# Kernel optimization log

Hardware: AMD Instinct MI355X
Metric: run time of the kernel (lower is better)

## Reference

```python
import jax, jax.numpy as jnp
import numpy as np

HEADS = 8
DIM_HEAD = 64
DIM = 512
MAX_POS_EMB = 512
SCALE = DIM_HEAD ** -0.5


def setup_inputs() -> dict:
    key = jax.random.key(0)
    ks = jax.random.split(key, 6)
    B, N = 2, 2048
    inner = HEADS * DIM_HEAD  # 512
    x = jax.random.normal(ks[0], (B, N, DIM), dtype=jnp.float32)
    # torch Linear weights stored as [out, in]; we keep [in, out] for x @ W
    Wq = jax.random.normal(ks[1], (DIM, inner), dtype=jnp.float32) * (DIM ** -0.5)
    Wkv = jax.random.normal(ks[2], (DIM, 2 * inner), dtype=jnp.float32) * (DIM ** -0.5)
    Wo = jax.random.normal(ks[3], (inner, DIM), dtype=jnp.float32) * (inner ** -0.5)
    bo = jax.random.normal(ks[4], (DIM,), dtype=jnp.float32) * 0.02
    rel_emb = jax.random.normal(ks[5], (2 * MAX_POS_EMB + 1, DIM_HEAD), dtype=jnp.float32)
    return {"x": x, "Wq": Wq, "Wkv": Wkv, "Wo": Wo, "bo": bo, "rel_emb": rel_emb}


def reference(x, Wq, Wkv, Wo, bo, rel_emb):
    B, N, _ = x.shape
    h, d = HEADS, DIM_HEAD
    q = x @ Wq                                # [B, N, h*d]
    kv = x @ Wkv                              # [B, N, 2*h*d]
    k, v = jnp.split(kv, 2, axis=-1)
    to_heads = lambda t: t.reshape(B, N, h, d).transpose(0, 2, 1, 3)  # [B, h, N, d]
    q, k, v = to_heads(q), to_heads(k), to_heads(v)

    dots = jnp.einsum('bhid,bhjd->bhij', q, k) * SCALE  # [B, h, N, N]

    # relative positional bias: dist clamped to [-max, max], shifted to [0, 2*max]
    seq = jnp.arange(N)
    dist = jnp.clip(seq[:, None] - seq[None, :], -MAX_POS_EMB, MAX_POS_EMB) + MAX_POS_EMB
    rel = rel_emb[dist]                                 # [N, N, d]
    pos_attn = jnp.einsum('bhnd,njd->bhnj', q, rel) * SCALE
    dots = dots + pos_attn

    attn = jax.nn.softmax(dots, axis=-1)
    out = jnp.einsum('bhij,bhjd->bhid', attn, v)        # [B, h, N, d]
    out = out.transpose(0, 2, 1, 3).reshape(B, N, h * d)
    return out @ Wo + bo
```

## Files before the change

kernel.cpp:

```cpp
#include <hip/hip_runtime.h>
#include <hip/hip_bf16.h>
#include <stdint.h>

#define HEADS 8
#define DHEAD 64
#define DIM 512
#define NSEQ 2048
#define BATCH 2
#define NROWS (BATCH * NSEQ)
#define QKV_N 1536
#define REL_ROWS 1025
#define REL_PITCH 1088
#define NSPLIT 2
#define KV_PER_SPLIT (NSEQ / NSPLIT)

static constexpr float SCALE_LOG2E = 0.125f * 1.4426950408889634f;

typedef __attribute__((ext_vector_type(8))) short bf16x8;
typedef __attribute__((ext_vector_type(4))) float f32x4;

__device__ __forceinline__ uint16_t f2bf(float f) {
    union { float f; uint32_t u; } v{f};
    uint32_t r = (v.u + 0x7FFFu + ((v.u >> 16) & 1u)) >> 16;
    return (uint16_t)r;
}
__device__ __forceinline__ float bf2f(uint16_t u) {
    union { uint32_t u; float f; } v{(uint32_t)u << 16};
    return v.f;
}

__global__ void prep_misc(const float* __restrict__ x, const float* __restrict__ rel,
                          uint16_t* __restrict__ xb, uint16_t* __restrict__ relb) {
    int total = NROWS * DIM + REL_PITCH * DHEAD;
    for (int idx = blockIdx.x * blockDim.x + threadIdx.x; idx < total; idx += gridDim.x * blockDim.x) {
        if (idx < NROWS * DIM) {
            xb[idx] = f2bf(x[idx]);
        } else {
            int i2 = idx - NROWS * DIM;
            relb[i2] = (i2 < REL_ROWS * DHEAD) ? f2bf(rel[i2]) : (uint16_t)0;
        }
    }
}

__global__ void prep_w(const float* __restrict__ Wq, const float* __restrict__ Wkv,
                       const float* __restrict__ Wo,
                       uint16_t* __restrict__ Wqkv_t, uint16_t* __restrict__ Wo_t) {
    __shared__ float tile[32][33];
    int bid = blockIdx.x;
    const float* src; uint16_t* dst; int J, ti, tj;
    if (bid < 256)      { src = Wq;  dst = Wqkv_t;             J = 512;  ti = bid >> 4;        tj = bid & 15; }
    else if (bid < 768) { int b = bid - 256; src = Wkv; dst = Wqkv_t + 512 * 512; J = 1024; ti = b >> 5; tj = b & 31; }
    else                { int b = bid - 768; src = Wo;  dst = Wo_t;   J = 512;  ti = b >> 4;        tj = b & 15; }
    int tx = threadIdx.x & 31, ty = threadIdx.x >> 5;
    int k0 = ti * 32, j0 = tj * 32;
    #pragma unroll
    for (int i = 0; i < 4; i++) tile[ty + 8 * i][tx] = src[(size_t)(k0 + ty + 8 * i) * J + j0 + tx];
    __syncthreads();
    #pragma unroll
    for (int i = 0; i < 4; i++) dst[(size_t)(j0 + ty + 8 * i) * 512 + k0 + tx] = f2bf(tile[tx][ty + 8 * i]);
}

template <bool BF16_OUT>
__global__ __launch_bounds__(256) void gemm128(const uint16_t* __restrict__ A,
                                               const uint16_t* __restrict__ Bt,
                                               void* __restrict__ Cout,
                                               const float* __restrict__ bias,
                                               int K, int ldc) {
    __shared__ char lds[32768];
    char* ldsA = lds;
    char* ldsB = lds + 16384;
    int m0 = blockIdx.x * 128, n0 = blockIdx.y * 128;
    int t = threadIdx.x, lane = t & 63, w = t >> 6;
    int wr = w >> 1, wc = w & 1;
    int l15 = lane & 15, lh = lane >> 4;
    f32x4 acc[4][4] = {};
    for (int k0 = 0; k0 < K; k0 += 64) {
        __syncthreads();
        {
            int row = t >> 3, ch = t & 7;
            #pragma unroll
            for (int p = 0; p < 4; p++) {
                int r = row + 32 * p;
                bf16x8 va = *(const bf16x8*)(A + (size_t)(m0 + r) * K + k0 + ch * 8);
                *(bf16x8*)(ldsA + r * 128 + ((ch * 16) ^ ((r & 7) << 4))) = va;
                bf16x8 vb = *(const bf16x8*)(Bt + (size_t)(n0 + r) * K + k0 + ch * 8);
                *(bf16x8*)(ldsB + r * 128 + ((ch * 16) ^ ((r & 7) << 4))) = vb;
            }
        }
        __syncthreads();
        #pragma unroll
        for (int kk = 0; kk < 2; kk++) {
            bf16x8 a[4], b[4];
            #pragma unroll
            for (int mi = 0; mi < 4; mi++) {
                int m = wr * 64 + mi * 16 + l15;
                a[mi] = *(const bf16x8*)(ldsA + m * 128 + ((kk * 64 + lh * 16) ^ ((m & 7) << 4)));
            }
            #pragma unroll
            for (int ni = 0; ni < 4; ni++) {
                int n = wc * 64 + ni * 16 + l15;
                b[ni] = *(const bf16x8*)(ldsB + n * 128 + ((kk * 64 + lh * 16) ^ ((n & 7) << 4)));
            }
            #pragma unroll
            for (int mi = 0; mi < 4; mi++)
                #pragma unroll
                for (int ni = 0; ni < 4; ni++)
                    acc[mi][ni] = __builtin_amdgcn_mfma_f32_16x16x32_bf16(a[mi], b[ni], acc[mi][ni], 0, 0, 0);
        }
    }
    #pragma unroll
    for (int mi = 0; mi < 4; mi++)
        #pragma unroll
        for (int ni = 0; ni < 4; ni++)
            #pragma unroll
            for (int i = 0; i < 4; i++) {
                int m = m0 + wr * 64 + mi * 16 + lh * 4 + i;
                int n = n0 + wc * 64 + ni * 16 + l15;
                float v = acc[mi][ni][i];
                if constexpr (BF16_OUT) ((uint16_t*)Cout)[(size_t)m * ldc + n] = f2bf(v);
                else                    ((float*)Cout)[(size_t)m * ldc + n] = v + bias[n];
            }
}

__global__ __launch_bounds__(256) void qrel_gemm(const uint16_t* __restrict__ QKV,
                                                 const uint16_t* __restrict__ relb,
                                                 uint16_t* __restrict__ qrel) {
    __shared__ char lds[16384];
    char* ldsA = lds;
    char* ldsB = lds + 8192;
    int h = blockIdx.y;
    int r0 = blockIdx.x * 64;
    int t = threadIdx.x, lane = t & 63, w = t >> 6;
    int l15 = lane & 15, lh = lane >> 4;
    {
        int row = t >> 3, ch = t & 7;
        #pragma unroll
        for (int p = 0; p < 2; p++) {
            int r = row + 32 * p;
            bf16x8 v = *(const bf16x8*)(QKV + (size_t)(r0 + r) * QKV_N + h * 64 + ch * 8);
            *(bf16x8*)(ldsA + r * 128 + ((ch * 16) ^ ((r & 7) << 4))) = v;
        }
    }
    __syncthreads();
    bf16x8 afrag[2];
    #pragma unroll
    for (int kk = 0; kk < 2; kk++) {
        int m = w * 16 + l15;
        afrag[kk] = *(const bf16x8*)(ldsA + m * 128 + ((kk * 64 + lh * 16) ^ ((m & 7) << 4)));
    }
    for (int pb = 0; pb < REL_PITCH / 64; pb++) {
        int p0 = pb * 64;
        __syncthreads();
        {
            int row = t >> 3, ch = t & 7;
            #pragma unroll
            for (int p = 0; p < 2; p++) {
                int r = row + 32 * p;
                bf16x8 v = *(const bf16x8*)(relb + (size_t)(p0 + r) * 64 + ch * 8);
                *(bf16x8*)(ldsB + r * 128 + ((ch * 16) ^ ((r & 7) << 4))) = v;
            }
        }
        __syncthreads();
        f32x4 acc[4] = {};
        #pragma unroll
        for (int kk = 0; kk < 2; kk++)
            #pragma unroll
            for (int ni = 0; ni < 4; ni++) {
                int n = ni * 16 + l15;
                bf16x8 b = *(const bf16x8*)(ldsB + n * 128 + ((kk * 64 + lh * 16) ^ ((n & 7) << 4)));
                acc[ni] = __builtin_amdgcn_mfma_f32_16x16x32_bf16(afrag[kk], b, acc[ni], 0, 0, 0);
            }
        #pragma unroll
        for (int ni = 0; ni < 4; ni++)
            #pragma unroll
            for (int i = 0; i < 4; i++) {
                int rr = r0 + w * 16 + lh * 4 + i;
                int p = p0 + ni * 16 + l15;
                qrel[((size_t)h * NROWS + rr) * REL_PITCH + p] = f2bf(acc[ni][i]);
            }
    }
}

__global__ __launch_bounds__(512, 4) void attn_kernel(const uint16_t* __restrict__ QKV,
                                                      const uint16_t* __restrict__ qrel,
                                                      float* __restrict__ Opart,
                                                      float* __restrict__ mlpart) {
    __shared__ char lds[53248];
    char* ldsQ = lds;
    char* ldsKV = lds + 16384;
    int qb = blockIdx.x, h = blockIdx.y;
    int b = blockIdx.z >> 1, sp = blockIdx.z & 1;
    int t = threadIdx.x, lane = t & 63, w = t >> 6;
    int l15 = lane & 15, lh = lane >> 4;
    int row = t >> 3, ch = t & 7;
    int n0 = qb * 128;
    int kvbase = sp * KV_PER_SPLIT;
    size_t rowQ = (size_t)b * NSEQ + n0;

    {
        int buf = t >> 8, idx = t & 255;
        uint32_t val = (idx < 16) ? 0x3F803F80u : 0u;
        char* p = ldsKV + buf * 18432 + 8192 + 8192 + (idx >> 4) * 128 + (idx & 15) * 8;
        *(uint32_t*)(p) = val;
        *(uint32_t*)(p + 4) = val;
    }

    #pragma unroll
    for (int p = 0; p < 2; p++) {
        int r = row + 64 * p;
        bf16x8 v = *(const bf16x8*)(QKV + (rowQ + r) * QKV_N + h * 64 + ch * 8);
        *(bf16x8*)(ldsQ + r * 128 + ((ch * 16) ^ ((r & 7) << 4))) = v;
    }
    __syncthreads();
    bf16x8 qf[2];
    #pragma unroll
    for (int kk = 0; kk < 2; kk++) {
        int m = w * 16 + l15;
        qf[kk] = *(const bf16x8*)(ldsQ + m * 128 + ((kk * 64 + lh * 16) ^ ((m & 7) << 4)));
    }
    char* myP = ldsQ + w * 2048;

    f32x4 oacc[5] = {};
    float mrow[4];
    #pragma unroll
    for (int i = 0; i < 4; i++) mrow[i] = -INFINITY;

    const uint16_t* qbase = qrel + ((size_t)h * NROWS + (size_t)b * NSEQ) * REL_PITCH;
    uint32_t rowbase[4];
    #pragma unroll
    for (int i = 0; i < 4; i++) rowbase[i] = (uint32_t)(n0 + w * 16 + lh * 4 + i) * REL_PITCH + 512;

    auto load_kv = [&](int tile, bf16x8& kr, bf16x8& vr) {
        size_t gro = ((size_t)b * NSEQ + kvbase + tile * 64 + row) * QKV_N + h * 64 + ch * 8;
        kr = *(const bf16x8*)(QKV + gro + 512);
        vr = *(const bf16x8*)(QKV + gro + 1024);
    };
    auto scatter_kv = [&](int tile, bf16x8& kr, bf16x8& vr) {
        char* ldsK = ldsKV + (tile & 1) * 18432;
        char* ldsV = ldsK + 8192;
        *(bf16x8*)(ldsK + row * 128 + ((ch * 16) ^ ((row & 7) << 4))) = kr;
        #pragma unroll
        for (int dd = 0; dd < 8; dd++) {
            int d = ch * 8 + dd;
            int s = dd ^ ch;
            *(uint16_t*)(ldsV + d * 128 + 2 * (row ^ (s << 3))) = (uint16_t)vr[dd];
        }
    };
    auto load_g = [&](int tile, uint16_t* g) {
        int kv0 = kvbase + tile * 64;
        int rel0 = n0 - kv0;
        if (rel0 <= -640) {
            #pragma unroll
            for (int i = 0; i < 4; i++) {
                uint16_t v = qbase[rowbase[i] - 512];
                #pragma unroll
                for (int nf = 0; nf < 4; nf++) g[nf * 4 + i] = v;
            }
        } else if (rel0 >= 576) {
            #pragma unroll
            for (int i = 0; i < 4; i++) {
                uint16_t v = qbase[rowbase[i] + 512];
                #pragma unroll
                for (int nf = 0; nf < 4; nf++) g[nf * 4 + i] = v;
            }
        } else {
            #pragma unroll
            for (int i = 0; i < 4; i++) {
                int nmk = (n0 + w * 16 + lh * 4 + i) - kv0;
                #pragma unroll
                for (int nf = 0; nf < 4; nf++) {
                    int d = nmk - (nf * 16 + l15);
                    d = d < -512 ? -512 : (d > 512 ? 512 : d);
                    g[nf * 4 + i] = qbase[rowbase[i] + d];
                }
            }
        }
    };

    const int NT = KV_PER_SPLIT / 64;
    uint16_t gA[16], gB[16];
    bf16x8 kreg, vreg;
    load_kv(0, kreg, vreg);
    load_g(0, gA);
    scatter_kv(0, kreg, vreg);

    auto body = [&](int tt, uint16_t* gCur, uint16_t* gNext) {
        char* ldsK = ldsKV + (tt & 1) * 18432;
        char* ldsV = ldsK + 8192;
        __syncthreads();
        bool pf = (tt + 1 < NT);
        if (pf) { load_kv(tt + 1, kreg, vreg); load_g(tt + 1, gNext); }

        f32x4 sacc[4] = {};
        __builtin_amdgcn_s_setprio(1);
        #pragma unroll
        for (int kk = 0; kk < 2; kk++)
            #pragma unroll
            for (int nf = 0; nf < 4; nf++) {
                int n = nf * 16 + l15;
                bf16x8 kfv = *(const bf16x8*)(ldsK + n * 128 + ((kk * 64 + lh * 16) ^ ((n & 7) << 4)));
                sacc[nf] = __builtin_amdgcn_mfma_f32_16x16x32_bf16(qf[kk], kfv, sacc[nf], 0, 0, 0);
            }
        __builtin_amdgcn_s_setprio(0);

        #pragma unroll
        for (int nf = 0; nf < 4; nf++)
            #pragma unroll
            for (int i = 0; i < 4; i++)
                sacc[nf][i] += bf2f(gCur[nf * 4 + i]);

        float lmax = sacc[0][0];
        #pragma unroll
        for (int nf = 0; nf < 4; nf++)
            #pragma unroll
            for (int i = 0; i < 4; i++) lmax = fmaxf(lmax, sacc[nf][i]);
        float mmin = fminf(fminf(mrow[0], mrow[1]), fminf(mrow[2], mrow[3]));
        if (!__all(lmax <= mmin + 64.0f)) {
            #pragma unroll
            for (int i = 0; i < 4; i++) {
                float mx = fmaxf(fmaxf(sacc[0][i], sacc[1][i]), fmaxf(sacc[2][i], sacc[3][i]));
                mx = fmaxf(mx, __shfl_xor(mx, 1));
                mx = fmaxf(mx, __shfl_xor(mx, 2));
                mx = fmaxf(mx, __shfl_xor(mx, 4));
                mx = fmaxf(mx, __shfl_xor(mx, 8));
                float mnew = fmaxf(mrow[i], mx);
                float alpha = exp2f((mrow[i] - mnew) * SCALE_LOG2E);
                mrow[i] = mnew;
                #pragma unroll
                for (int nf = 0; nf < 5; nf++) oacc[nf][i] *= alpha;
            }
        }

        #pragma unroll
        for (int i = 0; i < 4; i++) {
            int r = lh * 4 + i;
            int rsw = (r & 7) << 4;
            #pragma unroll
            for (int nf = 0; nf < 4; nf++) {
                float p = exp2f((sacc[nf][i] - mrow[i]) * SCALE_LOG2E);
                uint32_t pb;
                asm("v_cvt_pk_bf16_f32 %0, %1, %2" : "=v"(pb) : "v"(p), "v"(p));
                *(uint16_t*)(myP + r * 128 + (((nf * 16 + l15) * 2) ^ rsw)) = (uint16_t)pb;
            }
        }

        asm volatile("s_waitcnt lgkmcnt(0)" ::: "memory");
        __builtin_amdgcn_s_setprio(1);
        #pragma unroll
        for (int kk = 0; kk < 2; kk++) {
            bf16x8 pa = *(const bf16x8*)(myP + l15 * 128 + ((kk * 64 + lh * 16) ^ ((l15 & 7) << 4)));
            #pragma unroll
            for (int nf = 0; nf < 5; nf++) {
                int d = nf * 16 + l15;
                int sd = (d & 7) ^ ((d >> 3) & 7);
                bf16x8 vb = *(const bf16x8*)(ldsV + d * 128 + 16 * ((kk * 4 + lh) ^ sd));
                oacc[nf] = __builtin_amdgcn_mfma_f32_16x16x32_bf16(pa, vb, oacc[nf], 0, 0, 0);
            }
        }
        __builtin_amdgcn_s_setprio(0);
        if (pf) scatter_kv(tt + 1, kreg, vreg);
    };

    #pragma unroll 1
    for (int tt2 = 0; tt2 < NT; tt2 += 2) {
        body(tt2, gA, gB);
        body(tt2 + 1, gB, gA);
    }

    size_t rbase = ((size_t)(sp * BATCH + b) * HEADS + h) * NSEQ;
    #pragma unroll
    for (int nf = 0; nf < 4; nf++)
        #pragma unroll
        for (int i = 0; i < 4; i++) {
            int r = n0 + w * 16 + lh * 4 + i;
            Opart[(rbase + r) * 64 + nf * 16 + l15] = oacc[nf][i];
        }
    if (l15 == 0) {
        #pragma unroll
        for (int i = 0; i < 4; i++) {
            int r = n0 + w * 16 + lh * 4 + i;
            mlpart[(rbase + r) * 2]     = mrow[i];
            mlpart[(rbase + r) * 2 + 1] = oacc[4][i];
        }
    }
}

__global__ __launch_bounds__(256) void combine_kernel(const float* __restrict__ Opart,
                                                      const float* __restrict__ mlpart,
                                                      uint16_t* __restrict__ attO) {
    int lane = threadIdx.x & 63;
    int R = blockIdx.x * 4 + (threadIdx.x >> 6);
    const int SPSTRIDE = BATCH * HEADS * NSEQ;
    float m1 = mlpart[(size_t)R * 2], l1 = mlpart[(size_t)R * 2 + 1];
    float m2 = mlpart[((size_t)SPSTRIDE + R) * 2], l2 = mlpart[((size_t)SPSTRIDE + R) * 2 + 1];
    float M = fmaxf(m1, m2);
    float w1 = exp2f((m1 - M) * SCALE_LOG2E);
    float w2 = exp2f((m2 - M) * SCALE_LOG2E);
    float Linv = 1.f / (l1 * w1 + l2 * w2);
    float o1 = Opart[(size_t)R * 64 + lane];
    float o2 = Opart[((size_t)SPSTRIDE + R) * 64 + lane];
    float o = (o1 * w1 + o2 * w2) * Linv;
    int bh = R >> 11, n = R & 2047;
    int b = bh >> 3, hh = bh & 7;
    attO[((size_t)(b * NSEQ + n)) * DIM + hh * 64 + lane] = f2bf(o);
}

extern "C" void kernel_launch(void* const* d_in, const int* in_sizes, int n_in,
                              void* d_out, int out_size, void* d_ws, size_t ws_size,
                              hipStream_t stream) {
    const float* x   = (const float*)d_in[0];
    const float* Wq  = (const float*)d_in[1];
    const float* Wkv = (const float*)d_in[2];
    const float* Wo  = (const float*)d_in[3];
    const float* bo  = (const float*)d_in[4];
    const float* rel = (const float*)d_in[5];
    char* ws = (char*)d_ws;
    uint16_t* Xb     = (uint16_t*)(ws);
    float*    mlp    = (float*)(ws);
    uint16_t* Wqkv_t = (uint16_t*)(ws + 4194304);
    uint16_t* Wo_t   = (uint16_t*)(ws + 5767168);
    uint16_t* relb   = (uint16_t*)(ws + 6291456);
    uint16_t* QKV    = (uint16_t*)(ws + 6430720);
    uint16_t* attO   = (uint16_t*)(ws + 19013632);
    uint16_t* qrel   = (uint16_t*)(ws + 23207936);
    float*    Opart  = (float*)(ws + 94511104);

    prep_misc<<<2048, 256, 0, stream>>>(x, rel, Xb, relb);
    prep_w<<<1024, 256, 0, stream>>>(Wq, Wkv, Wo, Wqkv_t, Wo_t);
    gemm128<true><<<dim3(32, 12), 256, 0, stream>>>(Xb, Wqkv_t, QKV, nullptr, 512, QKV_N);
    qrel_gemm<<<dim3(64, 8), 256, 0, stream>>>(QKV, relb, qrel);
    attn_kernel<<<dim3(16, 8, 4), 512, 0, stream>>>(QKV, qrel, Opart, mlp);
    combine_kernel<<<8192, 256, 0, stream>>>(Opart, mlp, attO);
    gemm128<false><<<dim3(32, 4), 256, 0, stream>>>(attO, Wo_t, (float*)d_out, bo, 512, DIM);
}
```

Before: 159.5 us.

## Restructure attention kernel: smaller blocks, staged rel-bias window in LDS, XCD-aware block remap

The attention kernel drops from 128-row/512-thread blocks to 64-row/256-thread blocks, doubling grid size, and remaps block indices so neighbouring blocks are grouped per XCD. The relative-position bias, previously gathered per element from global memory with scalar loads, is now loaded as a contiguous vectorized window per query row into LDS and read back from there. K/V double buffering is replaced by single buffering with an extra barrier per tile, which trades reduced LDS use for more synchronisation.

```diff
diff --git a/kernel.cpp b/kernel.cpp
--- a/kernel.cpp
+++ b/kernel.cpp
@@ -181,35 +181,42 @@
     }
 }
 
-__global__ __launch_bounds__(512, 4) void attn_kernel(const uint16_t* __restrict__ QKV,
+__global__ __launch_bounds__(256, 4) void attn_kernel(const uint16_t* __restrict__ QKV,
                                                       const uint16_t* __restrict__ qrel,
                                                       float* __restrict__ Opart,
                                                       float* __restrict__ mlpart) {
-    __shared__ char lds[53248];
+    __shared__ __align__(16) char lds[35328];
     char* ldsQ = lds;
-    char* ldsKV = lds + 16384;
-    int qb = blockIdx.x, h = blockIdx.y;
-    int b = blockIdx.z >> 1, sp = blockIdx.z & 1;
+    char* ldsK = lds + 8192;
+    char* ldsV = lds + 16384;
+    char* ldsW = lds + 26624;
+
+    int flat = blockIdx.x + 32 * (blockIdx.y + 8 * blockIdx.z);
+    int x = (flat & 7) * 128 + (flat >> 3);
+    int qb = x & 31, h = (x >> 5) & 7, z = x >> 8;
+    int b = z >> 1, sp = z & 1;
+
     int t = threadIdx.x, lane = t & 63, w = t >> 6;
     int l15 = lane & 15, lh = lane >> 4;
-    int row = t >> 3, ch = t & 7;
-    int n0 = qb * 128;
+    int r4 = t >> 2, q4 = t & 3;
+    int n0 = qb * 64;
     int kvbase = sp * KV_PER_SPLIT;
-    size_t rowQ = (size_t)b * NSEQ + n0;
 
     {
-        int buf = t >> 8, idx = t & 255;
-        uint32_t val = (idx < 16) ? 0x3F803F80u : 0u;
-        char* p = ldsKV + buf * 18432 + 8192 + 8192 + (idx >> 4) * 128 + (idx & 15) * 8;
-        *(uint32_t*)(p) = val;
-        *(uint32_t*)(p + 4) = val;
-    }
-
-    #pragma unroll
-    for (int p = 0; p < 2; p++) {
-        int r = row + 64 * p;
-        bf16x8 v = *(const bf16x8*)(QKV + (rowQ + r) * QKV_N + h * 64 + ch * 8);
-        *(bf16x8*)(ldsQ + r * 128 + ((ch * 16) ^ ((r & 7) << 4))) = v;
+        int rr = t >> 4, e = t & 15;
+        uint32_t val = (rr == 0) ? 0x3F803F80u : 0u;
+        *(uint32_t*)(ldsV + 8192 + rr * 128 + e * 8)     = val;
+        *(uint32_t*)(ldsV + 8192 + rr * 128 + e * 8 + 4) = val;
+    }
+
+    {
+        size_t rowQ = (size_t)b * NSEQ + n0;
+        const uint16_t* src = QKV + (rowQ + r4) * QKV_N + h * 64 + q4 * 16;
+        bf16x8 v0 = *(const bf16x8*)(src);
+        bf16x8 v1 = *(const bf16x8*)(src + 8);
+        int sw = (r4 & 7) << 4;
+        *(bf16x8*)(ldsQ + r4 * 128 + ((q4 * 32) ^ sw))      = v0;
+        *(bf16x8*)(ldsQ + r4 * 128 + ((q4 * 32 + 16) ^ sw)) = v1;
     }
     __syncthreads();
     bf16x8 qf[2];
@@ -225,71 +232,72 @@
     #pragma unroll
     for (int i = 0; i < 4; i++) mrow[i] = -INFINITY;
 
-    const uint16_t* qbase = qrel + ((size_t)h * NROWS + (size_t)b * NSEQ) * REL_PITCH;
-    uint32_t rowbase[4];
-    #pragma unroll
-    for (int i = 0; i < 4; i++) rowbase[i] = (uint32_t)(n0 + w * 16 + lh * 4 + i) * REL_PITCH + 512;
-
-    auto load_kv = [&](int tile, bf16x8& kr, bf16x8& vr) {
-        size_t gro = ((size_t)b * NSEQ + kvbase + tile * 64 + row) * QKV_N + h * 64 + ch * 8;
-        kr = *(const bf16x8*)(QKV + gro + 512);
-        vr = *(const bf16x8*)(QKV + gro + 1024);
+    const uint16_t* gK = QKV + ((size_t)b * NSEQ + kvbase + r4) * QKV_N + 512 + h * 64 + q4 * 16;
+    const uint16_t* gV = gK + 512;
+    const uint16_t* qrow_n = qrel + ((size_t)h * NROWS + (size_t)b * NSEQ + n0 + r4) * REL_PITCH + 512;
+
+    bf16x8 kr[2], vr[2], wr[2];
+    auto load_kv = [&](int tile) {
+        size_t off = (size_t)tile * 64 * QKV_N;
+        kr[0] = *(const bf16x8*)(gK + off);
+        kr[1] = *(const bf16x8*)(gK + off + 8);
+        vr[0] = *(const bf16x8*)(gV + off);
+        vr[1] = *(const bf16x8*)(gV + off + 8);
     };
-    auto scatter_kv = [&](int tile, bf16x8& kr, bf16x8& vr) {
-        char* ldsK = ldsKV + (tile & 1) * 18432;
-        char* ldsV = ldsK + 8192;
-        *(bf16x8*)(ldsK + row * 128 + ((ch * 16) ^ ((row & 7) << 4))) = kr;
-        #pragma unroll
-        for (int dd = 0; dd < 8; dd++) {
-            int d = ch * 8 + dd;
-            int s = dd ^ ch;
-            *(uint16_t*)(ldsV + d * 128 + 2 * (row ^ (s << 3))) = (uint16_t)vr[dd];
+    auto load_w = [&](int tile) {
+        int kv0 = kvbase + tile * 64;
+        int base = (n0 + r4) - kv0 - 63;
+        #pragma unroll
+        for (int p = 0; p < 2; p++) {
+            int dlo = base + q4 * 16 + p * 8;
+            if (dlo >= -512 && dlo <= 505) {
+                wr[p] = *(const bf16x8*)(qrow_n + dlo);
+            } else {
+                #pragma unroll
+                for (int e = 0; e < 8; e++) {
+                    int d = dlo + e;
+                    d = d < -512 ? -512 : (d > 512 ? 512 : d);
+                    wr[p][e] = (short)qrow_n[d];
+                }
+            }
         }
     };
-    auto load_g = [&](int tile, uint16_t* g) {
-        int kv0 = kvbase + tile * 64;
-        int rel0 = n0 - kv0;
-        if (rel0 <= -640) {
-            #pragma unroll
-            for (int i = 0; i < 4; i++) {
-                uint16_t v = qbase[rowbase[i] - 512];
-                #pragma unroll
-                for (int nf = 0; nf < 4; nf++) g[nf * 4 + i] = v;
-            }
-        } else if (rel0 >= 576) {
-            #pragma unroll
-            for (int i = 0; i < 4; i++) {
-                uint16_t v = qbase[rowbase[i] + 512];
-                #pragma unroll
-                for (int nf = 0; nf < 4; nf++) g[nf * 4 + i] = v;
-            }
-        } else {
-            #pragma unroll
-            for (int i = 0; i < 4; i++) {
-                int nmk = (n0 + w * 16 + lh * 4 + i) - kv0;
-                #pragma unroll
-                for (int nf = 0; nf < 4; nf++) {
-                    int d = nmk - (nf * 16 + l15);
-                    d = d < -512 ? -512 : (d > 512 ? 512 : d);
-                    g[nf * 4 + i] = qbase[rowbase[i] + d];
-                }
-            }
-        }
+    auto scatter_all = [&]() {
+        int sw = (r4 & 7) << 4;
+        #pragma unroll
+        for (int p = 0; p < 2; p++)
+            *(bf16x8*)(ldsK + r4 * 128 + ((q4 * 32 + 16 * p) ^ sw)) = kr[p];
+        #pragma unroll
+        for (int p = 0; p < 2; p++)
+            #pragma unroll
+            for (int dd = 0; dd < 8; dd++) {
+                int d = q4 * 16 + p * 8 + dd;
+                int sd = (d & 7) ^ ((d >> 3) & 7);
+                *(uint16_t*)(ldsV + d * 128 + 2 * (r4 ^ (sd << 3))) = (uint16_t)vr[p][dd];
+            }
+        #pragma unroll
+        for (int p = 0; p < 2; p++)
+            *(bf16x8*)(ldsW + r4 * 136 + (q4 * 16 + p * 8) * 2) = wr[p];
     };
 
     const int NT = KV_PER_SPLIT / 64;
-    uint16_t gA[16], gB[16];
-    bf16x8 kreg, vreg;
-    load_kv(0, kreg, vreg);
-    load_g(0, gA);
-    scatter_kv(0, kreg, vreg);
-
-    auto body = [&](int tt, uint16_t* gCur, uint16_t* gNext) {
-        char* ldsK = ldsKV + (tt & 1) * 18432;
-        char* ldsV = ldsK + 8192;
+    load_kv(0);
+    load_w(0);
+    scatter_all();
+
+    #pragma unroll 1
+    for (int tt = 0; tt < NT; ++tt) {
         __syncthreads();
         bool pf = (tt + 1 < NT);
-        if (pf) { load_kv(tt + 1, kreg, vreg); load_g(tt + 1, gNext); }
+        if (pf) { load_kv(tt + 1); load_w(tt + 1); }
+
+        uint16_t gb[16];
+        #pragma unroll
+        for (int nf = 0; nf < 4; nf++)
+            #pragma unroll
+            for (int i = 0; i < 4; i++)
+                gb[nf * 4 + i] = *(const uint16_t*)(ldsW + (w * 16 + lh * 4 + i) * 136
+                                                    + (63 - nf * 16 - l15) * 2);
 
         f32x4 sacc[4] = {};
         __builtin_amdgcn_s_setprio(1);
@@ -307,7 +315,7 @@
         for (int nf = 0; nf < 4; nf++)
             #pragma unroll
             for (int i = 0; i < 4; i++)
-                sacc[nf][i] += bf2f(gCur[nf * 4 + i]);
+                sacc[nf][i] += bf2f(gb[nf * 4 + i]);
 
         float lmax = sacc[0][0];
         #pragma unroll
@@ -345,6 +353,7 @@
         }
 
         asm volatile("s_waitcnt lgkmcnt(0)" ::: "memory");
+        __builtin_amdgcn_sched_barrier(0);
         __builtin_amdgcn_s_setprio(1);
         #pragma unroll
         for (int kk = 0; kk < 2; kk++) {
@@ -358,13 +367,9 @@
             }
         }
         __builtin_amdgcn_s_setprio(0);
-        if (pf) scatter_kv(tt + 1, kreg, vreg);
-    };
-
-    #pragma unroll 1
-    for (int tt2 = 0; tt2 < NT; tt2 += 2) {
-        body(tt2, gA, gB);
-        body(tt2 + 1, gB, gA);
+
+        __syncthreads();
+        if (pf) scatter_all();
     }
 
     size_t rbase = ((size_t)(sp * BATCH + b) * HEADS + h) * NSEQ;
@@ -429,7 +434,7 @@
     prep_w<<<1024, 256, 0, stream>>>(Wq, Wkv, Wo, Wqkv_t, Wo_t);
     gemm128<true><<<dim3(32, 12), 256, 0, stream>>>(Xb, Wqkv_t, QKV, nullptr, 512, QKV_N);
     qrel_gemm<<<dim3(64, 8), 256, 0, stream>>>(QKV, relb, qrel);
-    attn_kernel<<<dim3(16, 8, 4), 512, 0, stream>>>(QKV, qrel, Opart, mlp);
+    attn_kernel<<<dim3(32, 8, 4), 256, 0, stream>>>(QKV, qrel, Opart, mlp);
     combine_kernel<<<8192, 256, 0, stream>>>(Opart, mlp, attO);
     gemm128<false><<<dim3(32, 4), 256, 0, stream>>>(attO, Wo_t, (float*)d_out, bo, 512, DIM);
 }
```

After: 261.3 us. 1.64x slower.

## Split attention KV into four parts, single-buffer LDS, raise occupancy, remap blocks

Applied to the files above, without the earlier changes.

Raises the KV split from 2 to 4, so the attention grid doubles to 1024 blocks, and the combine kernel now merges four partial results. The K/V LDS tiles go from double-buffered to single-buffered, with an extra barrier before the scatter, which cuts LDS per block so that six blocks per CU fit. Block indices are remapped so neighbouring blocks spread across heads and batches, and the gather of the positional bias for the next tile is moved after its current use. The cost is more partial-output traffic for combine, an extra sync per tile, and less overlap of KV loads with compute.

```diff
diff --git a/kernel.cpp b/kernel.cpp
--- a/kernel.cpp
+++ b/kernel.cpp
@@ -11,7 +11,7 @@
 #define QKV_N 1536
 #define REL_ROWS 1025
 #define REL_PITCH 1088
-#define NSPLIT 2
+#define NSPLIT 4
 #define KV_PER_SPLIT (NSEQ / NSPLIT)
 
 static constexpr float SCALE_LOG2E = 0.125f * 1.4426950408889634f;
@@ -181,15 +181,20 @@
     }
 }
 
-__global__ __launch_bounds__(512, 4) void attn_kernel(const uint16_t* __restrict__ QKV,
+__global__ __launch_bounds__(512, 6) void attn_kernel(const uint16_t* __restrict__ QKV,
                                                       const uint16_t* __restrict__ qrel,
                                                       float* __restrict__ Opart,
                                                       float* __restrict__ mlpart) {
-    __shared__ char lds[53248];
+    __shared__ __align__(16) char lds[34816];
     char* ldsQ = lds;
-    char* ldsKV = lds + 16384;
-    int qb = blockIdx.x, h = blockIdx.y;
-    int b = blockIdx.z >> 1, sp = blockIdx.z & 1;
+    char* ldsK = lds + 16384;
+    char* ldsV = lds + 24576;
+
+    int flat = blockIdx.x + 16 * (blockIdx.y + 8 * blockIdx.z);
+    int x = (flat & 7) * 128 + (flat >> 3);
+    int qb = x & 15, h = (x >> 4) & 7, z = x >> 7;
+    int b = z >> 2, sp = z & 3;
+
     int t = threadIdx.x, lane = t & 63, w = t >> 6;
     int l15 = lane & 15, lh = lane >> 4;
     int row = t >> 3, ch = t & 7;
@@ -197,10 +202,9 @@
     int kvbase = sp * KV_PER_SPLIT;
     size_t rowQ = (size_t)b * NSEQ + n0;
 
-    {
-        int buf = t >> 8, idx = t & 255;
-        uint32_t val = (idx < 16) ? 0x3F803F80u : 0u;
-        char* p = ldsKV + buf * 18432 + 8192 + 8192 + (idx >> 4) * 128 + (idx & 15) * 8;
+    if (t < 256) {
+        uint32_t val = ((t >> 4) == 0) ? 0x3F803F80u : 0u;
+        char* p = ldsV + 8192 + (t >> 4) * 128 + (t & 15) * 8;
         *(uint32_t*)(p) = val;
         *(uint32_t*)(p + 4) = val;
     }
@@ -235,9 +239,7 @@
         kr = *(const bf16x8*)(QKV + gro + 512);
         vr = *(const bf16x8*)(QKV + gro + 1024);
     };
-    auto scatter_kv = [&](int tile, bf16x8& kr, bf16x8& vr) {
-        char* ldsK = ldsKV + (tile & 1) * 18432;
-        char* ldsV = ldsK + 8192;
+    auto scatter_kv = [&](bf16x8& kr, bf16x8& vr) {
         *(bf16x8*)(ldsK + row * 128 + ((ch * 16) ^ ((row & 7) << 4))) = kr;
         #pragma unroll
         for (int dd = 0; dd < 8; dd++) {
@@ -278,18 +280,18 @@
     };
 
     const int NT = KV_PER_SPLIT / 64;
-    uint16_t gA[16], gB[16];
-    bf16x8 kreg, vreg;
-    load_kv(0, kreg, vreg);
-    load_g(0, gA);
-    scatter_kv(0, kreg, vreg);
-
-    auto body = [&](int tt, uint16_t* gCur, uint16_t* gNext) {
-        char* ldsK = ldsKV + (tt & 1) * 18432;
-        char* ldsV = ldsK + 8192;
+    uint16_t g[16];
+    bf16x8 kr, vr;
+
+    load_kv(0, kr, vr);
+    load_g(0, g);
+    scatter_kv(kr, vr);
+
+    #pragma unroll 1
+    for (int tt = 0; tt < NT; ++tt) {
         __syncthreads();
         bool pf = (tt + 1 < NT);
-        if (pf) { load_kv(tt + 1, kreg, vreg); load_g(tt + 1, gNext); }
+        if (pf) load_kv(tt + 1, kr, vr);
 
         f32x4 sacc[4] = {};
         __builtin_amdgcn_s_setprio(1);
@@ -307,7 +309,8 @@
         for (int nf = 0; nf < 4; nf++)
             #pragma unroll
             for (int i = 0; i < 4; i++)
-                sacc[nf][i] += bf2f(gCur[nf * 4 + i]);
+                sacc[nf][i] += bf2f(g[nf * 4 + i]);
+        if (pf) load_g(tt + 1, g);
 
         float lmax = sacc[0][0];
         #pragma unroll
@@ -345,6 +348,7 @@
         }
 
         asm volatile("s_waitcnt lgkmcnt(0)" ::: "memory");
+        __builtin_amdgcn_sched_barrier(0);
         __builtin_amdgcn_s_setprio(1);
         #pragma unroll
         for (int kk = 0; kk < 2; kk++) {
@@ -358,13 +362,9 @@
             }
         }
         __builtin_amdgcn_s_setprio(0);
-        if (pf) scatter_kv(tt + 1, kreg, vreg);
-    };
-
-    #pragma unroll 1
-    for (int tt2 = 0; tt2 < NT; tt2 += 2) {
-        body(tt2, gA, gB);
-        body(tt2 + 1, gB, gA);
+
+        __syncthreads();
+        if (pf) scatter_kv(kr, vr);
     }
 
     size_t rbase = ((size_t)(sp * BATCH + b) * HEADS + h) * NSEQ;
@@ -391,15 +391,21 @@
     int lane = threadIdx.x & 63;
     int R = blockIdx.x * 4 + (threadIdx.x >> 6);
     const int SPSTRIDE = BATCH * HEADS * NSEQ;
-    float m1 = mlpart[(size_t)R * 2], l1 = mlpart[(size_t)R * 2 + 1];
-    float m2 = mlpart[((size_t)SPSTRIDE + R) * 2], l2 = mlpart[((size_t)SPSTRIDE + R) * 2 + 1];
-    float M = fmaxf(m1, m2);
-    float w1 = exp2f((m1 - M) * SCALE_LOG2E);
-    float w2 = exp2f((m2 - M) * SCALE_LOG2E);
-    float Linv = 1.f / (l1 * w1 + l2 * w2);
-    float o1 = Opart[(size_t)R * 64 + lane];
-    float o2 = Opart[((size_t)SPSTRIDE + R) * 64 + lane];
-    float o = (o1 * w1 + o2 * w2) * Linv;
+    float m[NSPLIT], l[NSPLIT];
+    #pragma unroll
+    for (int s = 0; s < NSPLIT; s++) {
+        m[s] = mlpart[((size_t)s * SPSTRIDE + R) * 2];
+        l[s] = mlpart[((size_t)s * SPSTRIDE + R) * 2 + 1];
+    }
+    float M = fmaxf(fmaxf(m[0], m[1]), fmaxf(m[2], m[3]));
+    float acc = 0.f, den = 0.f;
+    #pragma unroll
+    for (int s = 0; s < NSPLIT; s++) {
+        float ws = exp2f((m[s] - M) * SCALE_LOG2E);
+        den += l[s] * ws;
+        acc += Opart[((size_t)s * SPSTRIDE + R) * 64 + lane] * ws;
+    }
+    float o = acc / den;
     int bh = R >> 11, n = R & 2047;
     int b = bh >> 3, hh = bh & 7;
     attO[((size_t)(b * NSEQ + n)) * DIM + hh * 64 + lane] = f2bf(o);
@@ -415,21 +421,21 @@
     const float* bo  = (const float*)d_in[4];
     const float* rel = (const float*)d_in[5];
     char* ws = (char*)d_ws;
-    uint16_t* Xb     = (uint16_t*)(ws);
     float*    mlp    = (float*)(ws);
-    uint16_t* Wqkv_t = (uint16_t*)(ws + 4194304);
-    uint16_t* Wo_t   = (uint16_t*)(ws + 5767168);
-    uint16_t* relb   = (uint16_t*)(ws + 6291456);
-    uint16_t* QKV    = (uint16_t*)(ws + 6430720);
-    uint16_t* attO   = (uint16_t*)(ws + 19013632);
-    uint16_t* qrel   = (uint16_t*)(ws + 23207936);
-    float*    Opart  = (float*)(ws + 94511104);
+    uint16_t* Wo_t   = (uint16_t*)(ws + 1048576);
+    uint16_t* attO   = (uint16_t*)(ws + 1572864);
+    uint16_t* QKV    = (uint16_t*)(ws + 5767168);
+    uint16_t* qrel   = (uint16_t*)(ws + 18350080);
+    float*    Opart  = (float*)(ws + 89653248);
+    uint16_t* Xb     = (uint16_t*)(ws + 89653248);
+    uint16_t* Wqkv_t = (uint16_t*)(ws + 93847552);
+    uint16_t* relb   = (uint16_t*)(ws + 95420416);
 
     prep_misc<<<2048, 256, 0, stream>>>(x, rel, Xb, relb);
     prep_w<<<1024, 256, 0, stream>>>(Wq, Wkv, Wo, Wqkv_t, Wo_t);
     gemm128<true><<<dim3(32, 12), 256, 0, stream>>>(Xb, Wqkv_t, QKV, nullptr, 512, QKV_N);
     qrel_gemm<<<dim3(64, 8), 256, 0, stream>>>(QKV, relb, qrel);
-    attn_kernel<<<dim3(16, 8, 4), 512, 0, stream>>>(QKV, qrel, Opart, mlp);
+    attn_kernel<<<dim3(16, 8, 8), 512, 0, stream>>>(QKV, qrel, Opart, mlp);
     combine_kernel<<<8192, 256, 0, stream>>>(Opart, mlp, attO);
     gemm128<false><<<dim3(32, 4), 256, 0, stream>>>(attO, Wo_t, (float*)d_out, bo, 512, DIM);
 }
```

New measurement: 331.4 us. 108% more time.
